# Kernel optimization log

Measured on AMD Instinct MI355X. Metric: run time of the kernel, lower is better.

## Reference

```python
import jax, jax.numpy as jnp
import numpy as np

S, B, D, H = 1024, 64, 1024, 1024


def setup_inputs() -> dict:
    key = jax.random.key(0)
    ks = jax.random.split(key, 18)
    stdv = 1.0 / np.sqrt(H)  # per reset_parameters
    inp = {"Xt": jax.random.normal(ks[0], (S, B, D), dtype=jnp.float32)}
    wnames = ["iiW", "hiW", "ifW", "hfW", "igW", "hgW", "ioW", "hoW"]
    bnames = ["iiB", "hiB", "ifB", "hfB", "igB", "hgB", "ioB", "hoB"]
    for i, n in enumerate(wnames):
        inp[n] = jax.random.uniform(ks[1 + i], (H, D if n[0] == "i" else H),
                                    minval=-stdv, maxval=stdv, dtype=jnp.float32)
    for i, n in enumerate(bnames):
        inp[n] = jax.random.uniform(ks[9 + i], (H,), minval=-stdv, maxval=stdv,
                                    dtype=jnp.float32)
    return inp


def reference(Xt, iiW, hiW, ifW, hfW, igW, hgW, ioW, hoW,
              iiB, hiB, ifB, hfB, igB, hgB, ioB, hoB):
    # single-layer LSTM, batch_first=False: scan over seq dim 0.
    # Math matches torch forward_one: separate input/hidden linears per gate,
    # actF = actC = tanh, dropout = 0.
    bias_i = iiB + hiB  # fuse constant bias sums once
    bias_f = ifB + hfB
    bias_g = igB + hgB
    bias_o = ioB + hoB

    def step(carry, x):
        h, c = carry  # [B, H] each
        I = jax.nn.sigmoid(x @ iiW.T + h @ hiW.T + bias_i)
        F = jax.nn.sigmoid(x @ ifW.T + h @ hfW.T + bias_f)
        G = jnp.tanh(x @ igW.T + h @ hgW.T + bias_g)
        O = jax.nn.sigmoid(x @ ioW.T + h @ hoW.T + bias_o)
        c_ = F * c + I * G
        y = O * jnp.tanh(c_)
        return (y, c_), y

    h0 = jnp.zeros((Xt.shape[1], hiW.shape[0]), dtype=Xt.dtype)
    c0 = jnp.zeros_like(h0)
    (hT, cT), Yt = jax.lax.scan(step, (h0, c0), Xt)
    return Yt, hT, cT  # stack_output=True -> Yt is [S, B, H]
```

## Files before the change

### kernel.cpp

```cpp
#include <hip/hip_runtime.h>
#include <hip/hip_bf16.h>
#include <stdint.h>


typedef __attribute__((ext_vector_type(8))) short bf16x8;
typedef __attribute__((ext_vector_type(4))) float f32x4;

__device__ __forceinline__ unsigned short f2bf(float f) {
    unsigned u = __builtin_bit_cast(unsigned, f);
    return (unsigned short)((u + 0x7fffu + ((u >> 16) & 1u)) >> 16);
}
__device__ __forceinline__ float fast_sigmoid(float x) {
    return __builtin_amdgcn_rcpf(1.f + __expf(-x));
}
__device__ __forceinline__ float fast_tanh(float x) {
    float xc = fminf(fmaxf(x, -9.f), 9.f);
    float e = __expf(2.f * xc);
    return (e - 1.f) * __builtin_amdgcn_rcpf(e + 1.f);
}

__global__ void init_kernel(const float* __restrict__ iiB, const float* __restrict__ hiB,
                            const float* __restrict__ ifB, const float* __restrict__ hfB,
                            const float* __restrict__ igB, const float* __restrict__ hgB,
                            const float* __restrict__ ioB, const float* __restrict__ hoB,
                            float* __restrict__ bias, unsigned short* __restrict__ hbuf0,
                            float* __restrict__ c_ws, unsigned int* __restrict__ bar) {
    int tid = blockIdx.x * 256 + threadIdx.x;
    if (tid < 128) bar[tid] = 0u;
    if (tid < 4096) {
        int g = tid >> 10, j = tid & 1023;
        const float* ib = (g == 0 ? iiB : g == 1 ? ifB : g == 2 ? igB : ioB);
        const float* hb = (g == 0 ? hiB : g == 1 ? hfB : g == 2 ? hgB : hoB);
        bias[tid] = ib[j] + hb[j];
    }
    for (int i = tid; i < 65536; i += 16384) {
        __hip_atomic_store(hbuf0 + i, (unsigned short)0, __ATOMIC_RELAXED, __HIP_MEMORY_SCOPE_AGENT);
        c_ws[i] = 0.f;
    }
}

__global__ void prep_weights(const float* __restrict__ iiW, const float* __restrict__ hiW,
                             const float* __restrict__ ifW, const float* __restrict__ hfW,
                             const float* __restrict__ igW, const float* __restrict__ hgW,
                             const float* __restrict__ ioW, const float* __restrict__ hoW,
                             unsigned short* __restrict__ Wx, unsigned short* __restrict__ Wh) {
    int n = blockIdx.x;
    int g = n >> 10, j = n & 1023;
    const float* wx = (g == 0 ? iiW : g == 1 ? ifW : g == 2 ? igW : ioW) + (size_t)j * 1024;
    const float* wh = (g == 0 ? hiW : g == 1 ? hfW : g == 2 ? hgW : hoW) + (size_t)j * 1024;
    int k = threadIdx.x * 4;
    float4 a = *(const float4*)(wx + k);
    float4 b = *(const float4*)(wh + k);
    ushort4 ra = { f2bf(a.x), f2bf(a.y), f2bf(a.z), f2bf(a.w) };
    ushort4 rb = { f2bf(b.x), f2bf(b.y), f2bf(b.z), f2bf(b.w) };
    *(ushort4*)(Wx + (size_t)n * 1024 + k) = ra;
    *(ushort4*)(Wh + (size_t)n * 1024 + k) = rb;
}

__global__ __launch_bounds__(256, 2) void xproj_gemm(const float* __restrict__ A,
                                                     const unsigned short* __restrict__ Wx,
                                                     const float* __restrict__ bias,
                                                     float* __restrict__ C) {
    __shared__ __align__(16) unsigned short Asm[128 * 32];
    __shared__ __align__(16) unsigned short Bsm[128 * 32];
    int tid = threadIdx.x;
    int lane = tid & 63, wv = tid >> 6;
    int l15 = lane & 15, l4 = lane >> 4;
    int wrow = wv >> 1, wcol = wv & 1;
    int bn0 = blockIdx.x * 128, bm0 = blockIdx.y * 128;
    f32x4 acc[4][4] = {};

    for (int kk = 0; kk < 32; ++kk) {
        int k0 = kk * 32;
        __syncthreads();
#pragma unroll
        for (int it = 0; it < 2; ++it) {
            int tau = it * 256 + tid;
            int row = tau >> 2, slot = tau & 3;
            const float* src = A + (size_t)(bm0 + row) * 1024 + k0 + slot * 8;
            float4 x0 = *(const float4*)src;
            float4 x1 = *(const float4*)(src + 4);
            bf16x8 pk;
            pk[0] = (short)f2bf(x0.x); pk[1] = (short)f2bf(x0.y);
            pk[2] = (short)f2bf(x0.z); pk[3] = (short)f2bf(x0.w);
            pk[4] = (short)f2bf(x1.x); pk[5] = (short)f2bf(x1.y);
            pk[6] = (short)f2bf(x1.z); pk[7] = (short)f2bf(x1.w);
            int dslot = slot ^ (row & 3);
            *(bf16x8*)((char*)Asm + row * 64 + dslot * 16) = pk;
        }
#pragma unroll
        for (int it = 0; it < 2; ++it) {
            int tau = it * 256 + tid;
            int row = tau >> 2, slot = tau & 3;
            int sslot = slot ^ (row & 3);
            const unsigned short* src = Wx + (size_t)(bn0 + row) * 1024 + k0 + sslot * 8;
            char* ldsb = (char*)Bsm + it * 4096 + wv * 1024;
            __builtin_amdgcn_global_load_lds((const __attribute__((address_space(1))) void*)src,
                                             (__attribute__((address_space(3))) void*)ldsb, 16, 0, 0);
        }
        __syncthreads();
        bf16x8 af[4], bfv[4];
#pragma unroll
        for (int i = 0; i < 4; ++i) {
            int rowa = wrow * 64 + i * 16 + l15;
            int sa = l4 ^ (rowa & 3);
            af[i] = *(const bf16x8*)((const char*)Asm + rowa * 64 + sa * 16);
            int rowb = wcol * 64 + i * 16 + l15;
            int sb = l4 ^ (rowb & 3);
            bfv[i] = *(const bf16x8*)((const char*)Bsm + rowb * 64 + sb * 16);
        }
#pragma unroll
        for (int i = 0; i < 4; ++i)
#pragma unroll
            for (int j = 0; j < 4; ++j)
                acc[i][j] = __builtin_amdgcn_mfma_f32_16x16x32_bf16(af[i], bfv[j], acc[i][j], 0, 0, 0);
    }
#pragma unroll
    for (int i = 0; i < 4; ++i) {
        int m = bm0 + wrow * 64 + i * 16 + l4 * 4;
#pragma unroll
        for (int j = 0; j < 4; ++j) {
            int n = bn0 + wcol * 64 + j * 16 + l15;
            int col = (n & 1023) * 4 + (n >> 10);
            float bs = bias[n];
#pragma unroll
            for (int r = 0; r < 4; ++r)
                C[(size_t)(m + r) * 4096 + col] = acc[i][j][r] + bs;
        }
    }
}

__global__ __launch_bounds__(256, 1) void lstm_steps(const float* __restrict__ xproj,
                                                     unsigned short* __restrict__ hbuf,
                                                     float* __restrict__ c_ws,
                                                     const unsigned short* __restrict__ Wh,
                                                     unsigned int* __restrict__ bar,
                                                     float* __restrict__ out,
                                                     int t0, int T) {
    __shared__ float red[8192];
    int tid = threadIdx.x, lane = tid & 63, wv = tid >> 6;
    int l15 = lane & 15, l4 = lane >> 4;
    int wg = blockIdx.x;
    int mhalf = wg & 1;
    int cg = wg >> 1;
    int j0 = cg * 16;
    unsigned int* mybar = bar + mhalf * 32;

    bf16x8 w[8][4];
#pragma unroll
    for (int ks = 0; ks < 8; ++ks)
#pragma unroll
        for (int g = 0; g < 4; ++g) {
            int n = g * 1024 + j0 + l15;
            int k = wv * 256 + ks * 32 + l4 * 8;
            w[ks][g] = *(const bf16x8*)(Wh + (size_t)n * 1024 + k);
        }
#pragma unroll
    for (int ks = 0; ks < 8; ++ks)
#pragma unroll
        for (int g = 0; g < 4; ++g)
            asm volatile("" : "+a"(w[ks][g]));

    float c_reg[2];
    int bq[2];
#pragma unroll
    for (int pi = 0; pi < 2; ++pi) {
        int p = wv * 2 + pi, m = p >> 2, r = p & 3;
        bq[pi] = mhalf * 32 + m * 16 + l4 * 4 + r;
        c_reg[pi] = c_ws[(size_t)bq[pi] * 1024 + j0 + l15];
    }

    float4 xp_cur[2];
#pragma unroll
    for (int pi = 0; pi < 2; ++pi)
        xp_cur[pi] = *(const float4*)(xproj + (size_t)bq[pi] * 4096 + (j0 + l15) * 4);

    for (int tl = 0; tl < T; ++tl) {
        int ts = t0 + tl;
        int par = ts & 1;
        const unsigned short* hb = hbuf + (size_t)par * 65536;

        bf16x8 af[2][8];
#pragma unroll
        for (int m = 0; m < 2; ++m) {
            int row = mhalf * 32 + m * 16 + l15;
            const unsigned short* rp = hb + (size_t)row * 1024 + wv * 256 + l4 * 8;
#pragma unroll
            for (int ks = 0; ks < 8; ++ks) {
                unsigned long long* p = (unsigned long long*)(rp + ks * 32);
                union { unsigned long long q[2]; bf16x8 v; } u;
                u.q[0] = __hip_atomic_load(p,     __ATOMIC_RELAXED, __HIP_MEMORY_SCOPE_AGENT);
                u.q[1] = __hip_atomic_load(p + 1, __ATOMIC_RELAXED, __HIP_MEMORY_SCOPE_AGENT);
                af[m][ks] = u.v;
            }
        }

        f32x4 acc[2][4] = {};
#pragma unroll
        for (int ks = 0; ks < 8; ++ks)
#pragma unroll
            for (int m = 0; m < 2; ++m)
#pragma unroll
                for (int g = 0; g < 4; ++g)
                    acc[m][g] = __builtin_amdgcn_mfma_f32_16x16x32_bf16(af[m][ks], w[ks][g], acc[m][g], 0, 0, 0);

#pragma unroll
        for (int m = 0; m < 2; ++m)
#pragma unroll
            for (int g = 0; g < 4; ++g)
#pragma unroll
                for (int r = 0; r < 4; ++r)
                    red[(wv * 32 + m * 16 + g * 4 + r) * 64 + lane] = acc[m][g][r];
        __syncthreads();

        float yv[2];
#pragma unroll
        for (int pi = 0; pi < 2; ++pi) {
            int p = wv * 2 + pi, m = p >> 2, r = p & 3;
            int b = bq[pi];
            int j = j0 + l15;
            const float* xpf = (const float*)&xp_cur[pi];
            float pre[4];
#pragma unroll
            for (int g = 0; g < 4; ++g) {
                int s = m * 16 + g * 4 + r;
                pre[g] = red[s * 64 + lane] + red[(32 + s) * 64 + lane] +
                         red[(64 + s) * 64 + lane] + red[(96 + s) * 64 + lane] + xpf[g];
            }
            float I = fast_sigmoid(pre[0]);
            float F = fast_sigmoid(pre[1]);
            float G = fast_tanh(pre[2]);
            float O = fast_sigmoid(pre[3]);
            float c = F * c_reg[pi] + I * G;
            c_reg[pi] = c;
            float y = O * fast_tanh(c);
            yv[pi] = y;
            __hip_atomic_store(hbuf + (size_t)(par ^ 1) * 65536 + (size_t)b * 1024 + j,
                               f2bf(y), __ATOMIC_RELAXED, __HIP_MEMORY_SCOPE_AGENT);
        }

        __syncthreads();

        int tln = (tl + 1 < T) ? tl + 1 : tl;
        float4 xp_nxt[2];
#pragma unroll
        for (int pi = 0; pi < 2; ++pi)
            xp_nxt[pi] = *(const float4*)(xproj + (size_t)(tln * 64 + bq[pi]) * 4096 + (j0 + l15) * 4);

        if (tid == 0) {
            __hip_atomic_fetch_add(mybar, 1u, __ATOMIC_RELAXED, __HIP_MEMORY_SCOPE_AGENT);
            unsigned target = (unsigned)(ts + 1) * 64u;
            while (__hip_atomic_load(mybar, __ATOMIC_RELAXED, __HIP_MEMORY_SCOPE_AGENT) < target)
                __builtin_amdgcn_s_sleep(1);
        }
        __syncthreads();

#pragma unroll
        for (int pi = 0; pi < 2; ++pi) {
            int b = bq[pi];
            int j = j0 + l15;
            out[(size_t)(ts * 64 + b) * 1024 + j] = yv[pi];
            if (ts == 1023) {
                out[67108864u + (size_t)b * 1024 + j] = yv[pi];
                out[67108864u + 65536u + (size_t)b * 1024 + j] = c_reg[pi];
            }
        }
        xp_cur[0] = xp_nxt[0];
        xp_cur[1] = xp_nxt[1];
    }
#pragma unroll
    for (int pi = 0; pi < 2; ++pi)
        c_ws[(size_t)bq[pi] * 1024 + j0 + l15] = c_reg[pi];
}

extern "C" void kernel_launch(void* const* d_in, const int* in_sizes, int n_in,
                              void* d_out, int out_size, void* d_ws, size_t ws_size,
                              hipStream_t stream) {
    (void)in_sizes; (void)n_in; (void)out_size;
    const float* Xt = (const float*)d_in[0];
    const float* W[8]; for (int i = 0; i < 8; ++i) W[i] = (const float*)d_in[1 + i];
    const float* Bv[8]; for (int i = 0; i < 8; ++i) Bv[i] = (const float*)d_in[9 + i];
    float* out = (float*)d_out;
    uint8_t* ws = (uint8_t*)d_ws;

    unsigned int*  bar   = (unsigned int*)(ws + 0);
    float*         bias  = (float*)(ws + 512);
    unsigned short* hbuf = (unsigned short*)(ws + 16896);
    float*         c_ws  = (float*)(ws + 279040);
    unsigned short* Wx   = (unsigned short*)(ws + 541184);
    unsigned short* Wh   = (unsigned short*)(ws + 8929792);
    float*         xproj = (float*)(ws + 17318400);

    size_t avail = ws_size > 17318400 ? ws_size - 17318400 : 0;
    int T = 4;
    for (int t = 1024; t >= 4; t >>= 1)
        if ((size_t)t * 1048576ull <= avail) { T = t; break; }

    init_kernel<<<64, 256, 0, stream>>>(Bv[0], Bv[1], Bv[2], Bv[3], Bv[4], Bv[5], Bv[6], Bv[7],
                                        bias, hbuf, c_ws, bar);
    prep_weights<<<4096, 256, 0, stream>>>(W[0], W[1], W[2], W[3], W[4], W[5], W[6], W[7], Wx, Wh);

    int nch = 1024 / T;
    for (int c = 0; c < nch; ++c) {
        xproj_gemm<<<dim3(32, T / 2), 256, 0, stream>>>(Xt + (size_t)c * T * 65536, Wx, bias, xproj);
        lstm_steps<<<128, 256, 0, stream>>>(xproj, hbuf, c_ws, Wh, bar, out, c * T, T);
    }
}
```

Before: 7.184 ms.

## Replace atomic counter barrier with per-workgroup flags and defer output stores

```diff
diff --git a/kernel.cpp b/kernel.cpp
--- a/kernel.cpp
+++ b/kernel.cpp
@@ -134,7 +134,7 @@
                                                      unsigned short* __restrict__ hbuf,
                                                      float* __restrict__ c_ws,
                                                      const unsigned short* __restrict__ Wh,
-                                                     unsigned int* __restrict__ bar,
+                                                     unsigned int* __restrict__ flags,
                                                      float* __restrict__ out,
                                                      int t0, int T) {
     __shared__ float red[8192];
@@ -144,7 +144,7 @@
     int mhalf = wg & 1;
     int cg = wg >> 1;
     int j0 = cg * 16;
-    unsigned int* mybar = bar + mhalf * 32;
+    unsigned int* myflags = flags + mhalf * 64;
 
     bf16x8 w[8][4];
 #pragma unroll
@@ -170,15 +170,27 @@
         c_reg[pi] = c_ws[(size_t)bq[pi] * 1024 + j0 + l15];
     }
 
-    float4 xp_cur[2];
+    float4 xp_cur[2], xp_nxt[2];
 #pragma unroll
     for (int pi = 0; pi < 2; ++pi)
         xp_cur[pi] = *(const float4*)(xproj + (size_t)bq[pi] * 4096 + (j0 + l15) * 4);
+
+    float yv[2] = {0.f, 0.f};
 
     for (int tl = 0; tl < T; ++tl) {
         int ts = t0 + tl;
         int par = ts & 1;
         const unsigned short* hb = hbuf + (size_t)par * 65536;
+
+        if (tl > 0) {
+#pragma unroll
+            for (int pi = 0; pi < 2; ++pi)
+                out[(size_t)((ts - 1) * 64 + bq[pi]) * 1024 + j0 + l15] = yv[pi];
+        }
+        int tln = (tl + 1 < T) ? tl + 1 : tl;
+#pragma unroll
+        for (int pi = 0; pi < 2; ++pi)
+            xp_nxt[pi] = *(const float4*)(xproj + (size_t)(tln * 64 + bq[pi]) * 4096 + (j0 + l15) * 4);
 
         bf16x8 af[2][8];
 #pragma unroll
@@ -213,7 +225,6 @@
                     red[(wv * 32 + m * 16 + g * 4 + r) * 64 + lane] = acc[m][g][r];
         __syncthreads();
 
-        float yv[2];
 #pragma unroll
         for (int pi = 0; pi < 2; ++pi) {
             int p = wv * 2 + pi, m = p >> 2, r = p & 3;
@@ -240,37 +251,34 @@
         }
 
         __syncthreads();
-
-        int tln = (tl + 1 < T) ? tl + 1 : tl;
-        float4 xp_nxt[2];
-#pragma unroll
-        for (int pi = 0; pi < 2; ++pi)
-            xp_nxt[pi] = *(const float4*)(xproj + (size_t)(tln * 64 + bq[pi]) * 4096 + (j0 + l15) * 4);
-
-        if (tid == 0) {
-            __hip_atomic_fetch_add(mybar, 1u, __ATOMIC_RELAXED, __HIP_MEMORY_SCOPE_AGENT);
-            unsigned target = (unsigned)(ts + 1) * 64u;
-            while (__hip_atomic_load(mybar, __ATOMIC_RELAXED, __HIP_MEMORY_SCOPE_AGENT) < target)
+        if (tid == 0)
+            __hip_atomic_store(myflags + cg, (unsigned)(ts + 1),
+                               __ATOMIC_RELAXED, __HIP_MEMORY_SCOPE_AGENT);
+        if (wv == 0) {
+            unsigned tgt = (unsigned)(ts + 1);
+            for (;;) {
+                unsigned f = __hip_atomic_load(myflags + lane, __ATOMIC_RELAXED,
+                                               __HIP_MEMORY_SCOPE_AGENT);
+                if (__ballot(f >= tgt) == ~0ull) break;
                 __builtin_amdgcn_s_sleep(1);
-        }
-        __syncthreads();
-
-#pragma unroll
-        for (int pi = 0; pi < 2; ++pi) {
-            int b = bq[pi];
-            int j = j0 + l15;
-            out[(size_t)(ts * 64 + b) * 1024 + j] = yv[pi];
-            if (ts == 1023) {
-                out[67108864u + (size_t)b * 1024 + j] = yv[pi];
-                out[67108864u + 65536u + (size_t)b * 1024 + j] = c_reg[pi];
             }
         }
+        __syncthreads();
+
         xp_cur[0] = xp_nxt[0];
         xp_cur[1] = xp_nxt[1];
     }
 #pragma unroll
-    for (int pi = 0; pi < 2; ++pi)
-        c_ws[(size_t)bq[pi] * 1024 + j0 + l15] = c_reg[pi];
+    for (int pi = 0; pi < 2; ++pi) {
+        int b = bq[pi];
+        int j = j0 + l15;
+        out[(size_t)((t0 + T - 1) * 64 + b) * 1024 + j] = yv[pi];
+        if (t0 + T == 1024) {
+            out[67108864u + (size_t)b * 1024 + j] = yv[pi];
+            out[67108864u + 65536u + (size_t)b * 1024 + j] = c_reg[pi];
+        }
+        c_ws[(size_t)b * 1024 + j0 + l15] = c_reg[pi];
+    }
 }
 
 extern "C" void kernel_launch(void* const* d_in, const int* in_sizes, int n_in,
```

Result: slower. 8.379 ms (+16.6%).

## Pipeline LSTM recurrence across four batch chunks with per-chunk barriers

Applied to the files above, without the earlier changes.

```diff
diff --git a/kernel.cpp b/kernel.cpp
--- a/kernel.cpp
+++ b/kernel.cpp
@@ -137,14 +137,12 @@
                                                      unsigned int* __restrict__ bar,
                                                      float* __restrict__ out,
                                                      int t0, int T) {
-    __shared__ float red[8192];
-    int tid = threadIdx.x, lane = tid & 63, wv = tid >> 6;
+    __shared__ float red[4160];
+    int tid = threadIdx.x, lane = tid & 63, kw = tid >> 6;
     int l15 = lane & 15, l4 = lane >> 4;
     int wg = blockIdx.x;
-    int mhalf = wg & 1;
-    int cg = wg >> 1;
-    int j0 = cg * 16;
-    unsigned int* mybar = bar + mhalf * 32;
+    int j0 = wg * 16;
+    int prow = tid >> 4, pj = tid & 15;
 
     bf16x8 w[8][4];
 #pragma unroll
@@ -152,7 +150,7 @@
 #pragma unroll
         for (int g = 0; g < 4; ++g) {
             int n = g * 1024 + j0 + l15;
-            int k = wv * 256 + ks * 32 + l4 * 8;
+            int k = kw * 256 + ks * 32 + l4 * 8;
             w[ks][g] = *(const bf16x8*)(Wh + (size_t)n * 1024 + k);
         }
 #pragma unroll
@@ -161,116 +159,106 @@
         for (int g = 0; g < 4; ++g)
             asm volatile("" : "+a"(w[ks][g]));
 
-    float c_reg[2];
-    int bq[2];
-#pragma unroll
-    for (int pi = 0; pi < 2; ++pi) {
-        int p = wv * 2 + pi, m = p >> 2, r = p & 3;
-        bq[pi] = mhalf * 32 + m * 16 + l4 * 4 + r;
-        c_reg[pi] = c_ws[(size_t)bq[pi] * 1024 + j0 + l15];
-    }
-
-    float4 xp_cur[2];
-#pragma unroll
-    for (int pi = 0; pi < 2; ++pi)
-        xp_cur[pi] = *(const float4*)(xproj + (size_t)bq[pi] * 4096 + (j0 + l15) * 4);
+    float c_reg[4], yv[4];
+    float4 xp_cur[4], xp_nxt[4];
+#pragma unroll
+    for (int c = 0; c < 4; ++c) {
+        int b = c * 16 + prow;
+        c_reg[c] = c_ws[(size_t)b * 1024 + j0 + pj];
+        xp_cur[c] = *(const float4*)(xproj + (size_t)b * 4096 + (j0 + pj) * 4);
+        yv[c] = 0.f;
+    }
 
     for (int tl = 0; tl < T; ++tl) {
         int ts = t0 + tl;
         int par = ts & 1;
         const unsigned short* hb = hbuf + (size_t)par * 65536;
-
-        bf16x8 af[2][8];
-#pragma unroll
-        for (int m = 0; m < 2; ++m) {
-            int row = mhalf * 32 + m * 16 + l15;
-            const unsigned short* rp = hb + (size_t)row * 1024 + wv * 256 + l4 * 8;
-#pragma unroll
-            for (int ks = 0; ks < 8; ++ks) {
-                unsigned long long* p = (unsigned long long*)(rp + ks * 32);
-                union { unsigned long long q[2]; bf16x8 v; } u;
-                u.q[0] = __hip_atomic_load(p,     __ATOMIC_RELAXED, __HIP_MEMORY_SCOPE_AGENT);
-                u.q[1] = __hip_atomic_load(p + 1, __ATOMIC_RELAXED, __HIP_MEMORY_SCOPE_AGENT);
-                af[m][ks] = u.v;
-            }
-        }
-
-        f32x4 acc[2][4] = {};
-#pragma unroll
-        for (int ks = 0; ks < 8; ++ks)
-#pragma unroll
-            for (int m = 0; m < 2; ++m)
+        unsigned short* hbn = hbuf + (size_t)(par ^ 1) * 65536;
+
+#pragma unroll
+        for (int c = 0; c < 4; ++c) {
+            if (tid == 0) {
+                unsigned tgt = (unsigned)ts * 64u;
+                while (__hip_atomic_load(bar + c * 32, __ATOMIC_RELAXED, __HIP_MEMORY_SCOPE_AGENT) < tgt)
+                    __builtin_amdgcn_s_sleep(1);
+            }
+            __syncthreads();
+
+            bf16x8 af[8];
+            {
+                const unsigned short* rp = hb + (size_t)(c * 16 + l15) * 1024 + kw * 256 + l4 * 8;
+#pragma unroll
+                for (int ks = 0; ks < 8; ++ks) {
+                    unsigned long long* p = (unsigned long long*)(rp + ks * 32);
+                    union { unsigned long long q[2]; bf16x8 v; } u;
+                    u.q[0] = __hip_atomic_load(p,     __ATOMIC_RELAXED, __HIP_MEMORY_SCOPE_AGENT);
+                    u.q[1] = __hip_atomic_load(p + 1, __ATOMIC_RELAXED, __HIP_MEMORY_SCOPE_AGENT);
+                    af[ks] = u.v;
+                }
+            }
+
+            f32x4 acc[4] = {};
+#pragma unroll
+            for (int ks = 0; ks < 8; ++ks)
 #pragma unroll
                 for (int g = 0; g < 4; ++g)
-                    acc[m][g] = __builtin_amdgcn_mfma_f32_16x16x32_bf16(af[m][ks], w[ks][g], acc[m][g], 0, 0, 0);
-
-#pragma unroll
-        for (int m = 0; m < 2; ++m)
+                    acc[g] = __builtin_amdgcn_mfma_f32_16x16x32_bf16(af[ks], w[ks][g], acc[g], 0, 0, 0);
+
 #pragma unroll
             for (int g = 0; g < 4; ++g)
 #pragma unroll
                 for (int r = 0; r < 4; ++r)
-                    red[(wv * 32 + m * 16 + g * 4 + r) * 64 + lane] = acc[m][g][r];
-        __syncthreads();
-
-        float yv[2];
-#pragma unroll
-        for (int pi = 0; pi < 2; ++pi) {
-            int p = wv * 2 + pi, m = p >> 2, r = p & 3;
-            int b = bq[pi];
-            int j = j0 + l15;
-            const float* xpf = (const float*)&xp_cur[pi];
-            float pre[4];
-#pragma unroll
-            for (int g = 0; g < 4; ++g) {
-                int s = m * 16 + g * 4 + r;
-                pre[g] = red[s * 64 + lane] + red[(32 + s) * 64 + lane] +
-                         red[(64 + s) * 64 + lane] + red[(96 + s) * 64 + lane] + xpf[g];
-            }
-            float I = fast_sigmoid(pre[0]);
-            float F = fast_sigmoid(pre[1]);
-            float G = fast_tanh(pre[2]);
-            float O = fast_sigmoid(pre[3]);
-            float c = F * c_reg[pi] + I * G;
-            c_reg[pi] = c;
-            float y = O * fast_tanh(c);
-            yv[pi] = y;
-            __hip_atomic_store(hbuf + (size_t)(par ^ 1) * 65536 + (size_t)b * 1024 + j,
-                               f2bf(y), __ATOMIC_RELAXED, __HIP_MEMORY_SCOPE_AGENT);
-        }
-
-        __syncthreads();
-
-        int tln = (tl + 1 < T) ? tl + 1 : tl;
-        float4 xp_nxt[2];
-#pragma unroll
-        for (int pi = 0; pi < 2; ++pi)
-            xp_nxt[pi] = *(const float4*)(xproj + (size_t)(tln * 64 + bq[pi]) * 4096 + (j0 + l15) * 4);
-
-        if (tid == 0) {
-            __hip_atomic_fetch_add(mybar, 1u, __ATOMIC_RELAXED, __HIP_MEMORY_SCOPE_AGENT);
-            unsigned target = (unsigned)(ts + 1) * 64u;
-            while (__hip_atomic_load(mybar, __ATOMIC_RELAXED, __HIP_MEMORY_SCOPE_AGENT) < target)
-                __builtin_amdgcn_s_sleep(1);
-        }
-        __syncthreads();
-
-#pragma unroll
-        for (int pi = 0; pi < 2; ++pi) {
-            int b = bq[pi];
-            int j = j0 + l15;
-            out[(size_t)(ts * 64 + b) * 1024 + j] = yv[pi];
-            if (ts == 1023) {
-                out[67108864u + (size_t)b * 1024 + j] = yv[pi];
-                out[67108864u + 65536u + (size_t)b * 1024 + j] = c_reg[pi];
-            }
-        }
-        xp_cur[0] = xp_nxt[0];
-        xp_cur[1] = xp_nxt[1];
-    }
-#pragma unroll
-    for (int pi = 0; pi < 2; ++pi)
-        c_ws[(size_t)bq[pi] * 1024 + j0 + l15] = c_reg[pi];
+                    red[(kw * 16 + g * 4 + r) * 65 + lane] = acc[g][r];
+            __syncthreads();
+
+            {
+                int b = c * 16 + prow;
+                int slot = (prow >> 2) * 16 + pj;
+                int rr = prow & 3;
+                const float* xpf = (const float*)&xp_cur[c];
+                float pre[4];
+#pragma unroll
+                for (int g = 0; g < 4; ++g)
+                    pre[g] = red[(0 * 16 + g * 4 + rr) * 65 + slot] +
+                             red[(1 * 16 + g * 4 + rr) * 65 + slot] +
+                             red[(2 * 16 + g * 4 + rr) * 65 + slot] +
+                             red[(3 * 16 + g * 4 + rr) * 65 + slot] + xpf[g];
+                float I = fast_sigmoid(pre[0]);
+                float F = fast_sigmoid(pre[1]);
+                float G = fast_tanh(pre[2]);
+                float O = fast_sigmoid(pre[3]);
+                float cc = F * c_reg[c] + I * G;
+                c_reg[c] = cc;
+                float y = O * fast_tanh(cc);
+                yv[c] = y;
+                __hip_atomic_store(hbn + (size_t)b * 1024 + j0 + pj, f2bf(y),
+                                   __ATOMIC_RELAXED, __HIP_MEMORY_SCOPE_AGENT);
+            }
+
+            __syncthreads();
+            if (tid == 0)
+                __hip_atomic_fetch_add(bar + c * 32, 1u, __ATOMIC_RELAXED, __HIP_MEMORY_SCOPE_AGENT);
+
+            {
+                int b = c * 16 + prow;
+                out[(size_t)(ts * 64 + b) * 1024 + j0 + pj] = yv[c];
+                int tln = (tl + 1 < T) ? tl + 1 : tl;
+                xp_nxt[c] = *(const float4*)(xproj + (size_t)(tln * 64 + b) * 4096 + (j0 + pj) * 4);
+            }
+        }
+#pragma unroll
+        for (int c = 0; c < 4; ++c) xp_cur[c] = xp_nxt[c];
+    }
+
+#pragma unroll
+    for (int c = 0; c < 4; ++c) {
+        int b = c * 16 + prow;
+        if (t0 + T == 1024) {
+            out[67108864u + (size_t)b * 1024 + j0 + pj] = yv[c];
+            out[67108864u + 65536u + (size_t)b * 1024 + j0 + pj] = c_reg[c];
+        }
+        c_ws[(size_t)b * 1024 + j0 + pj] = c_reg[c];
+    }
 }
 
 extern "C" void kernel_launch(void* const* d_in, const int* in_sizes, int n_in,
@@ -303,6 +291,6 @@
     int nch = 1024 / T;
     for (int c = 0; c < nch; ++c) {
         xproj_gemm<<<dim3(32, T / 2), 256, 0, stream>>>(Xt + (size_t)c * T * 65536, Wx, bias, xproj);
-        lstm_steps<<<128, 256, 0, stream>>>(xproj, hbuf, c_ws, Wh, bar, out, c * T, T);
-    }
-}
+        lstm_steps<<<64, 256, 0, stream>>>(xproj, hbuf, c_ws, Wh, bar, out, c * T, T);
+    }
+}
```

Measured after the change: 14.62 ms. 103% more time.
